# Optimization experiments

Measured on AMD Instinct MI355X. Metric: run time of the kernel, lower is better.

## Reference

```python
import jax, jax.numpy as jnp
import numpy as np


def setup_inputs() -> dict:
    key = jax.random.key(0)
    ks = jax.random.split(key, 6)
    T, B, N = 2048, 32, 1024
    return {
        "decoder_hx": jax.random.normal(ks[0], (B, N), dtype=jnp.float32),
        "encoder_outputs": jax.random.normal(ks[1], (T, B, N), dtype=jnp.float32),
        "encoder_feature": jax.random.normal(ks[2], (T, B, N), dtype=jnp.float32),
        "mask_tensor": jnp.ones((B, T), dtype=jnp.float32),
        "Ws_w": jax.random.normal(ks[3], (N, N), dtype=jnp.float32) / np.sqrt(N),
        "Ws_b": jnp.zeros((N,), dtype=jnp.float32),
        "v_w": jax.random.normal(ks[4], (1, N), dtype=jnp.float32) / np.sqrt(N),
        "v_b": jnp.zeros((1,), dtype=jnp.float32),
        "lin_w": jax.random.normal(ks[5], (N, 2 * N), dtype=jnp.float32) / np.sqrt(2 * N),
        "lin_b": jnp.zeros((N,), dtype=jnp.float32),
    }


def reference(decoder_hx, encoder_outputs, encoder_feature, mask_tensor,
              Ws_w, Ws_b, v_w, v_b, lin_w, lin_b):
    # Bahdanau additive attention.
    # dec_feature = W_s(decoder_hx): (b, n), broadcast over time t_k
    dec_feature = decoder_hx @ Ws_w.T + Ws_b                     # (b, n)
    e = jnp.tanh(encoder_feature + dec_feature[None, :, :])      # (t, b, n)
    # scores = v(e): rank-1 projection to a scalar per (t, b)
    scores = jnp.einsum('tbn,n->bt', e, v_w[0]) + v_b[0]         # (b, t)
    attn_dist = jax.nn.softmax(scores, axis=1) * mask_tensor     # (b, t)
    # weighted temporal sum of encoder outputs -> context vector
    content_vector = jnp.einsum('bt,tbn->bn', attn_dist, encoder_outputs)
    concat = jnp.concatenate([content_vector, decoder_hx], axis=1)  # (b, 2n)
    hx_attention = jnp.tanh(concat @ lin_w.T + lin_b)            # (b, n)
    return hx_attention
```

## Files before the change

kernel.cpp:

```cpp
#include <hip/hip_runtime.h>
#include <math.h>

#define T 2048
#define B 32
#define N 1024
#define NCHUNK 32
#define TCHUNK (T / NCHUNK)

__device__ __forceinline__ float fast_tanh(float x) {
    float e = __expf(2.0f * x);
    return 1.0f - 2.0f * __builtin_amdgcn_rcpf(e + 1.0f);
}

__device__ __forceinline__ float wave_reduce_sum(float v) {
    #pragma unroll
    for (int off = 32; off > 0; off >>= 1) v += __shfl_down(v, off, 64);
    return v;
}

__global__ void dec_feature_kernel(const float* __restrict__ hx,
                                   const float* __restrict__ Ws_w,
                                   const float* __restrict__ Ws_b,
                                   float* __restrict__ dec) {
    int w = blockIdx.x * 4 + (threadIdx.x >> 6);
    int lane = threadIdx.x & 63;
    int i = w >> 5;
    int b = w & 31;
    const float4* wr = (const float4*)(Ws_w + (size_t)i * N);
    const float4* hr = (const float4*)(hx + (size_t)b * N);
    float acc = 0.f;
    #pragma unroll
    for (int k = 0; k < 4; ++k) {
        float4 a = wr[k * 64 + lane];
        float4 h = hr[k * 64 + lane];
        acc += a.x * h.x + a.y * h.y + a.z * h.z + a.w * h.w;
    }
    acc = wave_reduce_sum(acc);
    if (lane == 0) dec[(size_t)b * N + i] = acc + Ws_b[i];
}

__global__ void scores_kernel(const float* __restrict__ ef,
                              const float* __restrict__ dec,
                              const float* __restrict__ v_w,
                              const float* __restrict__ v_b,
                              float* __restrict__ scores) {
    int bx = blockIdx.x;
    int b = bx & 31;
    int tq = bx >> 5;
    int wid = threadIdx.x >> 6;
    int lane = threadIdx.x & 63;
    int t = tq * 4 + wid;
    const float4* e4 = (const float4*)(ef + ((size_t)t * B + b) * N);
    const float4* d4 = (const float4*)(dec + (size_t)b * N);
    const float4* v4 = (const float4*)v_w;
    float acc = 0.f;
    #pragma unroll
    for (int k = 0; k < 4; ++k) {
        float4 e = e4[k * 64 + lane];
        float4 d = d4[k * 64 + lane];
        float4 v = v4[k * 64 + lane];
        acc += fast_tanh(e.x + d.x) * v.x + fast_tanh(e.y + d.y) * v.y
             + fast_tanh(e.z + d.z) * v.z + fast_tanh(e.w + d.w) * v.w;
    }
    acc = wave_reduce_sum(acc);
    if (lane == 0) scores[(size_t)b * T + t] = acc + v_b[0];
}

__global__ void content_partial_kernel(const float* __restrict__ eo,
                                       const float* __restrict__ scores,
                                       const float* __restrict__ mask,
                                       float* __restrict__ partial) {
    int b = blockIdx.y;
    int chunk = blockIdx.x;
    int tid = threadIdx.x;
    int lane = tid & 63, wid = tid >> 6;
    __shared__ float red[4];
    __shared__ float p_sh[TCHUNK];

    float s[8];
    float m = -1e30f;
    #pragma unroll
    for (int k = 0; k < 8; ++k) {
        s[k] = scores[(size_t)b * T + tid + k * 256];
        m = fmaxf(m, s[k]);
    }
    #pragma unroll
    for (int off = 32; off > 0; off >>= 1) m = fmaxf(m, __shfl_down(m, off, 64));
    if (lane == 0) red[wid] = m;
    __syncthreads();
    m = fmaxf(fmaxf(red[0], red[1]), fmaxf(red[2], red[3]));
    __syncthreads();

    float sum = 0.f;
    #pragma unroll
    for (int k = 0; k < 8; ++k) sum += __expf(s[k] - m);
    sum = wave_reduce_sum(sum);
    if (lane == 0) red[wid] = sum;
    __syncthreads();
    float invL = __builtin_amdgcn_rcpf(red[0] + red[1] + red[2] + red[3]);

    if (tid < TCHUNK) {
        int t = chunk * TCHUNK + tid;
        p_sh[tid] = __expf(scores[(size_t)b * T + t] - m) * invL
                  * mask[(size_t)b * T + t];
    }
    __syncthreads();

    const float4* base = (const float4*)eo;
    float4 acc = {0.f, 0.f, 0.f, 0.f};
    #pragma unroll 4
    for (int tt = 0; tt < TCHUNK; ++tt) {
        int t = chunk * TCHUNK + tt;
        float a = p_sh[tt];
        float4 e = base[((size_t)t * B + b) * (N / 4) + tid];
        acc.x += a * e.x; acc.y += a * e.y; acc.z += a * e.z; acc.w += a * e.w;
    }
    ((float4*)partial)[((size_t)chunk * B + b) * (N / 4) + tid] = acc;
}

__global__ void content_reduce_kernel(const float* __restrict__ partial,
                                      float* __restrict__ content) {
    int g = blockIdx.x * 256 + threadIdx.x;
    const float4* p4 = (const float4*)partial;
    float4 acc = {0.f, 0.f, 0.f, 0.f};
    #pragma unroll 8
    for (int c = 0; c < NCHUNK; ++c) {
        float4 v = p4[(size_t)c * (B * N / 4) + g];
        acc.x += v.x; acc.y += v.y; acc.z += v.z; acc.w += v.w;
    }
    ((float4*)content)[g] = acc;
}

__global__ void out_kernel(const float* __restrict__ content,
                           const float* __restrict__ hx,
                           const float* __restrict__ lin_w,
                           const float* __restrict__ lin_b,
                           float* __restrict__ out) {
    int w = blockIdx.x * 4 + (threadIdx.x >> 6);
    int lane = threadIdx.x & 63;
    int i = w >> 5;
    int b = w & 31;
    const float4* wr = (const float4*)(lin_w + (size_t)i * 2 * N);
    const float4* cr = (const float4*)(content + (size_t)b * N);
    const float4* hr = (const float4*)(hx + (size_t)b * N);
    float acc = 0.f;
    #pragma unroll
    for (int k = 0; k < 4; ++k) {
        float4 a = wr[k * 64 + lane];
        float4 c = cr[k * 64 + lane];
        acc += a.x * c.x + a.y * c.y + a.z * c.z + a.w * c.w;
    }
    #pragma unroll
    for (int k = 0; k < 4; ++k) {
        float4 a = wr[256 + k * 64 + lane];
        float4 h = hr[k * 64 + lane];
        acc += a.x * h.x + a.y * h.y + a.z * h.z + a.w * h.w;
    }
    acc = wave_reduce_sum(acc);
    if (lane == 0) out[(size_t)b * N + i] = fast_tanh(acc + lin_b[i]);
}

extern "C" void kernel_launch(void* const* d_in, const int* in_sizes, int n_in,
                              void* d_out, int out_size, void* d_ws, size_t ws_size,
                              hipStream_t stream) {
    const float* hx    = (const float*)d_in[0];
    const float* eo    = (const float*)d_in[1];
    const float* ef    = (const float*)d_in[2];
    const float* mask  = (const float*)d_in[3];
    const float* Ws_w  = (const float*)d_in[4];
    const float* Ws_b  = (const float*)d_in[5];
    const float* v_w   = (const float*)d_in[6];
    const float* v_b   = (const float*)d_in[7];
    const float* lin_w = (const float*)d_in[8];
    const float* lin_b = (const float*)d_in[9];
    float* out = (float*)d_out;

    float* ws      = (float*)d_ws;
    float* dec     = ws;
    float* scores  = dec + B * N;
    float* content = scores + B * T;
    float* partial = content + B * N;

    dec_feature_kernel<<<(B * N) / 4, 256, 0, stream>>>(hx, Ws_w, Ws_b, dec);
    scores_kernel<<<(T * B) / 4, 256, 0, stream>>>(ef, dec, v_w, v_b, scores);
    content_partial_kernel<<<dim3(NCHUNK, B), 256, 0, stream>>>(eo, scores, mask, partial);
    content_reduce_kernel<<<(B * N / 4) / 256, 256, 0, stream>>>(partial, content);
    out_kernel<<<(B * N) / 4, 256, 0, stream>>>(content, hx, lin_w, lin_b, out);
}
```

Before: 554.3 us.

## Fuse score computation into content kernel with split-softmax chunk statistics

The separate scores kernel goes away. Each (chunk, batch) block now computes its own 64 attention scores from encoder_feature, then a local max and exp-sum, and writes unnormalized weighted partial context vectors. The reduce kernel rescales each chunk's partial by exp(m_c - M) and divides by the global sum, in the style of flash-decoding. This drops the scores round trip, the redundant full-row softmax every block did, one launch, and the v_b add, which softmax ignores. The trade-off is that score work now runs in only 1024 blocks, with waves looping serially over rows, so there may be less memory-level parallelism than the old 16384-block scores kernel had.

```diff
diff --git a/kernel.cpp b/kernel.cpp
--- a/kernel.cpp
+++ b/kernel.cpp
@@ -39,70 +39,60 @@
     if (lane == 0) dec[(size_t)b * N + i] = acc + Ws_b[i];
 }
 
-__global__ void scores_kernel(const float* __restrict__ ef,
-                              const float* __restrict__ dec,
-                              const float* __restrict__ v_w,
-                              const float* __restrict__ v_b,
-                              float* __restrict__ scores) {
-    int bx = blockIdx.x;
-    int b = bx & 31;
-    int tq = bx >> 5;
-    int wid = threadIdx.x >> 6;
-    int lane = threadIdx.x & 63;
-    int t = tq * 4 + wid;
-    const float4* e4 = (const float4*)(ef + ((size_t)t * B + b) * N);
-    const float4* d4 = (const float4*)(dec + (size_t)b * N);
-    const float4* v4 = (const float4*)v_w;
-    float acc = 0.f;
-    #pragma unroll
-    for (int k = 0; k < 4; ++k) {
-        float4 e = e4[k * 64 + lane];
-        float4 d = d4[k * 64 + lane];
-        float4 v = v4[k * 64 + lane];
-        acc += fast_tanh(e.x + d.x) * v.x + fast_tanh(e.y + d.y) * v.y
-             + fast_tanh(e.z + d.z) * v.z + fast_tanh(e.w + d.w) * v.w;
-    }
-    acc = wave_reduce_sum(acc);
-    if (lane == 0) scores[(size_t)b * T + t] = acc + v_b[0];
-}
-
-__global__ void content_partial_kernel(const float* __restrict__ eo,
-                                       const float* __restrict__ scores,
-                                       const float* __restrict__ mask,
-                                       float* __restrict__ partial) {
+__global__ void score_content_kernel(const float* __restrict__ ef,
+                                     const float* __restrict__ eo,
+                                     const float* __restrict__ dec,
+                                     const float* __restrict__ v_w,
+                                     const float* __restrict__ mask,
+                                     float* __restrict__ partial,
+                                     float* __restrict__ mstat,
+                                     float* __restrict__ lstat) {
     int b = blockIdx.y;
     int chunk = blockIdx.x;
     int tid = threadIdx.x;
     int lane = tid & 63, wid = tid >> 6;
-    __shared__ float red[4];
+    __shared__ float s_sh[TCHUNK];
     __shared__ float p_sh[TCHUNK];
 
-    float s[8];
+    const float4* d4 = (const float4*)(dec + (size_t)b * N);
+    const float4* v4 = (const float4*)v_w;
+    float4 dreg[4], vreg[4];
+    #pragma unroll
+    for (int k = 0; k < 4; ++k) {
+        dreg[k] = d4[k * 64 + lane];
+        vreg[k] = v4[k * 64 + lane];
+    }
+
+    for (int tt = wid; tt < TCHUNK; tt += 4) {
+        int t = chunk * TCHUNK + tt;
+        const float4* e4 = (const float4*)(ef + ((size_t)t * B + b) * N);
+        float acc = 0.f;
+        #pragma unroll
+        for (int k = 0; k < 4; ++k) {
+            float4 e = e4[k * 64 + lane];
+            acc += fast_tanh(e.x + dreg[k].x) * vreg[k].x
+                 + fast_tanh(e.y + dreg[k].y) * vreg[k].y
+                 + fast_tanh(e.z + dreg[k].z) * vreg[k].z
+                 + fast_tanh(e.w + dreg[k].w) * vreg[k].w;
+        }
+        acc = wave_reduce_sum(acc);
+        if (lane == 0) s_sh[tt] = acc;
+    }
+    __syncthreads();
+
     float m = -1e30f;
     #pragma unroll
-    for (int k = 0; k < 8; ++k) {
-        s[k] = scores[(size_t)b * T + tid + k * 256];
-        m = fmaxf(m, s[k]);
-    }
-    #pragma unroll
-    for (int off = 32; off > 0; off >>= 1) m = fmaxf(m, __shfl_down(m, off, 64));
-    if (lane == 0) red[wid] = m;
-    __syncthreads();
-    m = fmaxf(fmaxf(red[0], red[1]), fmaxf(red[2], red[3]));
-    __syncthreads();
-
-    float sum = 0.f;
-    #pragma unroll
-    for (int k = 0; k < 8; ++k) sum += __expf(s[k] - m);
-    sum = wave_reduce_sum(sum);
-    if (lane == 0) red[wid] = sum;
-    __syncthreads();
-    float invL = __builtin_amdgcn_rcpf(red[0] + red[1] + red[2] + red[3]);
+    for (int tt = 0; tt < TCHUNK; ++tt) m = fmaxf(m, s_sh[tt]);
 
     if (tid < TCHUNK) {
         int t = chunk * TCHUNK + tid;
-        p_sh[tid] = __expf(scores[(size_t)b * T + t] - m) * invL
-                  * mask[(size_t)b * T + t];
+        float ex = __expf(s_sh[tid] - m);
+        p_sh[tid] = ex * mask[(size_t)b * T + t];
+        float l = wave_reduce_sum(ex);
+        if (tid == 0) {
+            mstat[chunk * B + b] = m;
+            lstat[chunk * B + b] = l;
+        }
     }
     __syncthreads();
 
@@ -119,15 +109,31 @@
 }
 
 __global__ void content_reduce_kernel(const float* __restrict__ partial,
+                                      const float* __restrict__ mstat,
+                                      const float* __restrict__ lstat,
                                       float* __restrict__ content) {
     int g = blockIdx.x * 256 + threadIdx.x;
+    int b = g >> 8;
+    float M = -1e30f;
+    #pragma unroll
+    for (int c = 0; c < NCHUNK; ++c) M = fmaxf(M, mstat[c * B + b]);
+    float w[NCHUNK];
+    float L = 0.f;
+    #pragma unroll
+    for (int c = 0; c < NCHUNK; ++c) {
+        w[c] = __expf(mstat[c * B + b] - M);
+        L += w[c] * lstat[c * B + b];
+    }
+    float invL = __builtin_amdgcn_rcpf(L);
     const float4* p4 = (const float4*)partial;
     float4 acc = {0.f, 0.f, 0.f, 0.f};
     #pragma unroll 8
     for (int c = 0; c < NCHUNK; ++c) {
         float4 v = p4[(size_t)c * (B * N / 4) + g];
-        acc.x += v.x; acc.y += v.y; acc.z += v.z; acc.w += v.w;
+        acc.x += w[c] * v.x; acc.y += w[c] * v.y;
+        acc.z += w[c] * v.z; acc.w += w[c] * v.w;
     }
+    acc.x *= invL; acc.y *= invL; acc.z *= invL; acc.w *= invL;
     ((float4*)content)[g] = acc;
 }
 
@@ -170,20 +176,21 @@
     const float* Ws_w  = (const float*)d_in[4];
     const float* Ws_b  = (const float*)d_in[5];
     const float* v_w   = (const float*)d_in[6];
-    const float* v_b   = (const float*)d_in[7];
     const float* lin_w = (const float*)d_in[8];
     const float* lin_b = (const float*)d_in[9];
     float* out = (float*)d_out;
 
     float* ws      = (float*)d_ws;
     float* dec     = ws;
-    float* scores  = dec + B * N;
-    float* content = scores + B * T;
+    float* mstat   = dec + B * N;
+    float* lstat   = mstat + NCHUNK * B;
+    float* content = lstat + NCHUNK * B;
     float* partial = content + B * N;
 
     dec_feature_kernel<<<(B * N) / 4, 256, 0, stream>>>(hx, Ws_w, Ws_b, dec);
-    scores_kernel<<<(T * B) / 4, 256, 0, stream>>>(ef, dec, v_w, v_b, scores);
-    content_partial_kernel<<<dim3(NCHUNK, B), 256, 0, stream>>>(eo, scores, mask, partial);
-    content_reduce_kernel<<<(B * N / 4) / 256, 256, 0, stream>>>(partial, content);
+    score_content_kernel<<<dim3(NCHUNK, B), 256, 0, stream>>>(
+        ef, eo, dec, v_w, mask, partial, mstat, lstat);
+    content_reduce_kernel<<<(B * N / 4) / 256, 256, 0, stream>>>(
+        partial, mstat, lstat, content);
     out_kernel<<<(B * N) / 4, 256, 0, stream>>>(content, hx, lin_w, lin_b, out);
 }
```

After: 558.5 us. Within noise of the previous version (+0.7%).
